# Kernel optimization log

Hardware: AMD Instinct MI355X
Metric: run time of the kernel (lower is better)

The kernel has to match this reference:

```python
import jax, jax.numpy as jnp
import numpy as np

EMB = 768
HEADS = 4
HEAD_DIM = EMB // HEADS


def setup_inputs() -> dict:
    key = jax.random.key(0)
    ks = jax.random.split(key, 11)
    B, S = 8, 2048
    scale = 1.0 / np.sqrt(EMB)
    inp = {
        "q": jax.random.normal(ks[0], (B, S, EMB), dtype=jnp.float32),
        "k": jax.random.normal(ks[1], (B, S, EMB), dtype=jnp.float32),
        "v": jax.random.normal(ks[2], (B, S, EMB), dtype=jnp.float32),
        "Wq": jax.random.normal(ks[3], (EMB, EMB), dtype=jnp.float32) * scale,
        "bq": jnp.zeros((EMB,), dtype=jnp.float32),
        "Wk": jax.random.normal(ks[4], (EMB, EMB), dtype=jnp.float32) * scale,
        "bk": jnp.zeros((EMB,), dtype=jnp.float32),
        "Wv": jax.random.normal(ks[5], (EMB, EMB), dtype=jnp.float32) * scale,
        "bv": jnp.zeros((EMB,), dtype=jnp.float32),
        "Wo": jax.random.normal(ks[6], (EMB, EMB), dtype=jnp.float32) * scale,
        "bo": jnp.zeros((EMB,), dtype=jnp.float32),
    }
    return inp


def reference(q, k, v, Wq, bq, Wk, bk, Wv, bv, Wo, bo):
    B, S, _ = q.shape
    # Linear projections (torch Linear: x @ W.T + b)
    Q = q @ Wq.T + bq
    K = k @ Wk.T + bk
    V = v @ Wv.T + bv
    # split heads: [B, H, S, Dh]
    def split(x):
        return x.reshape(B, S, HEADS, HEAD_DIM).transpose(0, 2, 1, 3)
    Qh, Kh, Vh = split(Q), split(K), split(V)
    # energy [B, H, S, S]; note: original's mask_fill is a non-inplace no-op, so no masking
    energy = jnp.einsum("bhqd,bhkd->bhqk", Qh, Kh)
    att = jax.nn.softmax(energy / jnp.sqrt(jnp.float32(HEAD_DIM)), axis=-1)
    # dropout p=0 -> identity
    out = jnp.einsum("bhqk,bhkd->bhqd", att, Vh)
    out = out.transpose(0, 2, 1, 3).reshape(B, S, EMB)
    return out @ Wo.T + bo
```

## Files before the change

kernel.cpp:

```cpp
#include <hip/hip_runtime.h>
#include <hip/hip_bf16.h>
#include <cstdint>
#include <cstddef>

#define EMB   768
#define HEADS 4
#define HD    192
#define BATCH 8
#define SEQ   2048
#define MROWS (BATCH * SEQ)

typedef __attribute__((ext_vector_type(8))) short bf16x8;
typedef __attribute__((ext_vector_type(4))) float f32x4;

#define GLOBAL_AS __attribute__((address_space(1)))
#define LDS_AS    __attribute__((address_space(3)))

__device__ __forceinline__ void async16(unsigned short* lds, const unsigned short* g) {
    __builtin_amdgcn_global_load_lds((const GLOBAL_AS void*)g, (LDS_AS void*)lds, 16, 0, 0);
}

__device__ __forceinline__ unsigned short f2bf(float f) {
    union { float f; unsigned int u; } v; v.f = f;
    unsigned int u = v.u;
    unsigned int r = u + 0x7fffu + ((u >> 16) & 1u);
    return (unsigned short)(r >> 16);
}

__device__ __forceinline__ unsigned long long pack4bf(float4 f) {
    union { __hip_bfloat162 h; unsigned int u; } a, b;
    a.h = __float22bfloat162_rn(make_float2(f.x, f.y));
    b.h = __float22bfloat162_rn(make_float2(f.z, f.w));
    return (unsigned long long)a.u | ((unsigned long long)b.u << 32);
}

__device__ __forceinline__ int swz(int colbyte, int row) {
    return colbyte ^ ((row & 7) << 4);
}

__global__ __launch_bounds__(256) void conv_kernel(
    const float* __restrict__ x, unsigned short* __restrict__ y, int n4)
{
    int i = blockIdx.x * 256 + threadIdx.x;
    int stride = gridDim.x * 256;
    for (; i < n4; i += stride) {
        float4 f = ((const float4*)x)[i];
        ((unsigned long long*)y)[i] = pack4bf(f);
    }
}

__global__ __launch_bounds__(256) void conv3_kernel(
    const float* __restrict__ a, const float* __restrict__ b,
    const float* __restrict__ c, unsigned short* __restrict__ y, int n4)
{
    int i = blockIdx.x * 256 + threadIdx.x;
    int stride = gridDim.x * 256;
    for (; i < 3 * n4; i += stride) {
        int sel = i / n4, off = i - sel * n4;
        const float* s = (sel == 0) ? a : (sel == 1) ? b : c;
        float4 f = ((const float4*)s)[off];
        ((unsigned long long*)y)[i] = pack4bf(f);
    }
}

#define GEMM_PROLOG                                                          \
    const int tid  = threadIdx.x;                                            \
    const int n0   = blockIdx.x * 128;                                       \
    const int m0   = blockIdx.y * 128;                                       \
    const int w    = tid >> 6;                                               \
    const int lane = tid & 63;                                               \
    const int l15  = lane & 15;                                              \
    const int quad = lane >> 4;                                              \
    const int wm   = (w >> 1) * 64;                                          \
    const int wn   = (w & 1) * 64;                                           \
    const int arow = lane >> 2;           \
    const int acol = (lane & 3) * 8;                  \
    f32x4 acc[4][4];                                                         \
    _Pragma("unroll")                                                        \
    for (int a = 0; a < 4; a++)                                              \
        _Pragma("unroll")                                                    \
        for (int b = 0; b < 4; b++) acc[a][b] = (f32x4)0.0f;

#define GEMM_KLOOP(Aptr, Bptr)                                               \
    for (int k0 = 0; k0 < 768; k0 += 32) {                                   \
        __syncthreads();                                                     \
        _Pragma("unroll")                                                    \
        for (int j = 0; j < 2; j++) {                                        \
            int r = w * 32 + j * 16 + arow;                                  \
            async16(&Al[(w * 2 + j) * 512],                                  \
                    Aptr + (size_t)(m0 + r) * 768 + k0 + acol);              \
            async16(&Bl[(w * 2 + j) * 512],                                  \
                    Bptr + (size_t)(n0 + r) * 768 + k0 + acol);              \
        }                                                                    \
        __syncthreads();                                                     \
        bf16x8 af[4], bfr[4];                                                \
        _Pragma("unroll")                                                    \
        for (int mi = 0; mi < 4; mi++)                                       \
            af[mi] = *(const bf16x8*)&Al[(wm + mi * 16 + l15) * 32 + quad * 8]; \
        _Pragma("unroll")                                                    \
        for (int ni = 0; ni < 4; ni++)                                       \
            bfr[ni] = *(const bf16x8*)&Bl[(wn + ni * 16 + l15) * 32 + quad * 8]; \
        _Pragma("unroll")                                                    \
        for (int mi = 0; mi < 4; mi++)                                       \
            _Pragma("unroll")                                                \
            for (int ni = 0; ni < 4; ni++)                                   \
                acc[mi][ni] = __builtin_amdgcn_mfma_f32_16x16x32_bf16(       \
                    af[mi], bfr[ni], acc[mi][ni], 0, 0, 0);                  \
    }

__global__ __launch_bounds__(256) void proj_kernel(
    const unsigned short* __restrict__ X,
    const unsigned short* __restrict__ Wb,
    const float* __restrict__ bias,
    unsigned short* __restrict__ out,
    float scale)
{
    __shared__ __align__(16) unsigned short Al[128 * 32];
    __shared__ __align__(16) unsigned short Bl[128 * 32];
    GEMM_PROLOG
    GEMM_KLOOP(X, Wb)

    const int b = m0 >> 11;
#pragma unroll
    for (int mi = 0; mi < 4; mi++) {
#pragma unroll
        for (int ni = 0; ni < 4; ni++) {
            int jj = n0 + wn + ni * 16 + l15;
            int h  = jj / HD;
            int d  = jj - h * HD;
            float bj = bias[jj];
#pragma unroll
            for (int r = 0; r < 4; r++) {
                int i = m0 + wm + mi * 16 + quad * 4 + r;
                int s = i & (SEQ - 1);
                out[(size_t)((b * HEADS + h) * SEQ + s) * HD + d] =
                    f2bf((acc[mi][ni][r] + bj) * scale);
            }
        }
    }
}

__global__ __launch_bounds__(256) void vproj_kernel(
    const unsigned short* __restrict__ X,
    const unsigned short* __restrict__ Wb,
    const float* __restrict__ bias,
    unsigned short* __restrict__ out)
{
    __shared__ __align__(16) unsigned short smem[8192];
    unsigned short* Al = smem;
    unsigned short* Bl = smem + 4096;
    GEMM_PROLOG
    GEMM_KLOOP(X, Wb)

    __syncthreads();
    unsigned short* Tl = smem;
    const int batch = m0 >> 11;
    const int s0    = m0 & (SEQ - 1);

#pragma unroll
    for (int g = 0; g < 4; g++) {
        if ((w & 1) == (g >> 1)) {
#pragma unroll
            for (int t = 0; t < 2; t++) {
                int ni = (g & 1) * 2 + t;
                int jj = n0 + (w & 1) * 64 + ni * 16 + l15;
                int dl = t * 16 + l15;
                float bj = bias[jj];
#pragma unroll
                for (int mi = 0; mi < 4; mi++)
#pragma unroll
                    for (int r = 0; r < 4; r++)
                        Tl[dl * 136 + wm + mi * 16 + quad * 4 + r] =
                            f2bf(acc[mi][ni][r] + bj);
            }
        }
        __syncthreads();
#pragma unroll
        for (int t = 0; t < 2; t++) {
            int u  = tid + t * 256;
            int dl = u >> 4;
            int cg = u & 15;
            int jj = n0 + g * 32 + dl;
            int hh = jj / HD;
            int d  = jj - hh * HD;
            *(int4*)(out + ((size_t)((batch * HEADS + hh) * HD + d)) * SEQ + s0 + cg * 8) =
                *(const int4*)&Tl[dl * 136 + cg * 8];
        }
        __syncthreads();
    }
}

__global__ __launch_bounds__(256) void oproj_kernel(
    const unsigned short* __restrict__ A,
    const unsigned short* __restrict__ Wb,
    const float* __restrict__ bias,
    float* __restrict__ out)
{
    __shared__ __align__(16) unsigned short Al[128 * 32];
    __shared__ __align__(16) unsigned short Bl[128 * 32];
    GEMM_PROLOG
    GEMM_KLOOP(A, Wb)

#pragma unroll
    for (int mi = 0; mi < 4; mi++) {
#pragma unroll
        for (int ni = 0; ni < 4; ni++) {
            int jj = n0 + wn + ni * 16 + l15;
            float bj = bias[jj];
#pragma unroll
            for (int r = 0; r < 4; r++) {
                int i = m0 + wm + mi * 16 + quad * 4 + r;
                out[(size_t)i * 768 + jj] = acc[mi][ni][r] + bj;
            }
        }
    }
}

__global__ __launch_bounds__(256, 2) void attn_kernel(
    const unsigned short* __restrict__ Q,
    const unsigned short* __restrict__ K,
    const unsigned short* __restrict__ Vt,
    unsigned short* __restrict__ O)
{
    __shared__ __align__(16) unsigned short Kl[64 * 192];
    __shared__ __align__(16) unsigned short Vl[192 * 64];
    __shared__ __align__(16) unsigned short Pl[4 * 32 * 64];

    const int tid  = threadIdx.x;
    const int w    = tid >> 6;
    const int lane = tid & 63;
    const int l15  = lane & 15;
    const int quad = lane >> 4;
    const int flat = blockIdx.x;
    const int loc  = flat >> 3;
    const int bh   = (flat & 7) * 4 + (loc >> 4);
    const int qt   = loc & 15;
    const int b    = bh >> 2;
    const int h    = bh & 3;
    const size_t kbase = (size_t)bh * SEQ * HD;

    bf16x8 qf[2][6];
    {
        const unsigned short* qp =
            Q + kbase + (size_t)(qt * 128 + w * 32 + l15) * HD + quad * 8;
#pragma unroll
        for (int mg = 0; mg < 2; mg++)
#pragma unroll
            for (int kk = 0; kk < 6; kk++)
                qf[mg][kk] = *(const bf16x8*)(qp + mg * 16 * HD + kk * 32);
    }

#pragma unroll
    for (int i = 0; i < 6; i++) {
        int u = tid + i * 256;
        int row = u / 24, rem = u - row * 24;
        int cgp = rem ^ (row & 7);
        async16(&Kl[(i * 256 + w * 64) * 8],
                K + kbase + (size_t)row * HD + cgp * 8);
    }

    f32x4 oacc[2][12];
#pragma unroll
    for (int mg = 0; mg < 2; mg++)
#pragma unroll
        for (int i = 0; i < 12; i++) oacc[mg][i] = (f32x4)0.0f;
    float lacc[2][4] = {{0.f, 0.f, 0.f, 0.f}, {0.f, 0.f, 0.f, 0.f}};

    for (int kt = 0; kt < SEQ / 64; kt++) {
        __syncthreads();

#pragma unroll
        for (int i = 0; i < 6; i++) {
            int u = tid + i * 256;
            int row = u >> 3;
            int cgp = (u & 7) ^ (row & 7);
            async16(&Vl[(i * 256 + w * 64) * 8],
                    Vt + kbase + (size_t)row * SEQ + kt * 64 + cgp * 8);
        }

        f32x4 sacc[2][4];
#pragma unroll
        for (int mg = 0; mg < 2; mg++)
#pragma unroll
            for (int nj = 0; nj < 4; nj++) sacc[mg][nj] = (f32x4)0.0f;

        __builtin_amdgcn_s_setprio(1);
#pragma unroll
        for (int kk = 0; kk < 6; kk++) {
#pragma unroll
            for (int nj = 0; nj < 4; nj++) {
                int row = nj * 16 + l15;
                bf16x8 bfr = *(const bf16x8*)((const char*)Kl + row * 384 +
                                              swz(kk * 64 + quad * 16, row));
                sacc[0][nj] = __builtin_amdgcn_mfma_f32_16x16x32_bf16(
                    qf[0][kk], bfr, sacc[0][nj], 0, 0, 0);
                sacc[1][nj] = __builtin_amdgcn_mfma_f32_16x16x32_bf16(
                    qf[1][kk], bfr, sacc[1][nj], 0, 0, 0);
            }
        }
        __builtin_amdgcn_s_setprio(0);

        {
            char* pw = (char*)Pl + w * 4096;
#pragma unroll
            for (int mg = 0; mg < 2; mg++)
#pragma unroll
                for (int nj = 0; nj < 4; nj++) {
                    int colb = (nj * 16 + l15) * 2;
#pragma unroll
                    for (int r = 0; r < 4; r++) {
                        float pv = __expf(sacc[mg][nj][r]);
                        lacc[mg][r] += pv;
                        int row = mg * 16 + quad * 4 + r;
                        *(unsigned short*)(pw + row * 128 + swz(colb, row)) = f2bf(pv);
                    }
                }
        }

        __syncthreads();

        {
            int ktn = (kt + 1) & (SEQ / 64 - 1);
#pragma unroll
            for (int i = 0; i < 6; i++) {
                int u = tid + i * 256;
                int row = u / 24, rem = u - row * 24;
                int cgp = rem ^ (row & 7);
                async16(&Kl[(i * 256 + w * 64) * 8],
                        K + kbase + (size_t)(ktn * 64 + row) * HD + cgp * 8);
            }
        }

#pragma unroll
        for (int kk = 0; kk < 2; kk++) {
            const char* pr = (const char*)Pl + w * 4096;
            bf16x8 pa0 = *(const bf16x8*)(pr + l15 * 128 + swz(kk * 64 + quad * 16, l15));
            bf16x8 pa1 = *(const bf16x8*)(pr + (16 + l15) * 128 + swz(kk * 64 + quad * 16, 16 + l15));
            __builtin_amdgcn_s_setprio(1);
#pragma unroll
            for (int nf = 0; nf < 12; nf++) {
                int vrow = nf * 16 + l15;
                bf16x8 vb = *(const bf16x8*)((const char*)Vl + vrow * 128 +
                                             swz(kk * 64 + quad * 16, vrow));
                oacc[0][nf] = __builtin_amdgcn_mfma_f32_16x16x32_bf16(pa0, vb, oacc[0][nf], 0, 0, 0);
                oacc[1][nf] = __builtin_amdgcn_mfma_f32_16x16x32_bf16(pa1, vb, oacc[1][nf], 0, 0, 0);
            }
            __builtin_amdgcn_s_setprio(0);
        }
    }

    float inv[2][4];
#pragma unroll
    for (int mg = 0; mg < 2; mg++)
#pragma unroll
        for (int r = 0; r < 4; r++) {
            float lsum = lacc[mg][r];
#pragma unroll
            for (int off = 1; off < 16; off <<= 1)
                lsum += __shfl_xor(lsum, off, 64);
            inv[mg][r] = 1.0f / lsum;
        }
#pragma unroll
    for (int mg = 0; mg < 2; mg++)
#pragma unroll
        for (int nf = 0; nf < 12; nf++) {
            int col = h * HD + nf * 16 + l15;
#pragma unroll
            for (int r = 0; r < 4; r++) {
                int s = qt * 128 + w * 32 + mg * 16 + quad * 4 + r;
                O[(size_t)(b * SEQ + s) * EMB + col] = f2bf(oacc[mg][nf][r] * inv[mg][r]);
            }
        }
}

extern "C" void kernel_launch(void* const* d_in, const int* in_sizes, int n_in,
                              void* d_out, int out_size, void* d_ws, size_t ws_size,
                              hipStream_t stream)
{
    const float* q  = (const float*)d_in[0];
    const float* k  = (const float*)d_in[1];
    const float* v  = (const float*)d_in[2];
    const float* Wq = (const float*)d_in[3];
    const float* bq = (const float*)d_in[4];
    const float* Wk = (const float*)d_in[5];
    const float* bk = (const float*)d_in[6];
    const float* Wv = (const float*)d_in[7];
    const float* bv = (const float*)d_in[8];
    const float* Wo = (const float*)d_in[9];
    const float* bo = (const float*)d_in[10];
    float* out = (float*)d_out;

    unsigned short* Xbf = (unsigned short*)d_out;
    unsigned short* S   = (unsigned short*)d_ws;
    unsigned short* Qb  = S  + (size_t)MROWS * EMB;
    unsigned short* Kb  = Qb + (size_t)MROWS * EMB;
    unsigned short* Vb  = Kb + (size_t)MROWS * EMB;
    const size_t WSZ = (size_t)EMB * EMB;

    const float scl = 0.07216878364870323f;
    const int   nx4 = MROWS * EMB / 4;
    const int   nw4 = EMB * EMB / 4;

    dim3 pb(256);
    dim3 pg(EMB / 128, MROWS / 128);
    dim3 cgx(4096), cgw(576);

    conv3_kernel<<<dim3(1728), pb, 0, stream>>>(Wq, Wk, Wv, S, nw4);

    conv_kernel<<<cgx, pb, 0, stream>>>(q, Xbf, nx4);
    proj_kernel<<<pg, pb, 0, stream>>>(Xbf, S, bq, Qb, scl);

    conv_kernel<<<cgx, pb, 0, stream>>>(k, Xbf, nx4);
    proj_kernel<<<pg, pb, 0, stream>>>(Xbf, S + WSZ, bk, Kb, 1.0f);

    conv_kernel<<<cgx, pb, 0, stream>>>(v, Xbf, nx4);
    vproj_kernel<<<pg, pb, 0, stream>>>(Xbf, S + 2 * WSZ, bv, Vb);

    dim3 ag(512);
    attn_kernel<<<ag, pb, 0, stream>>>(Qb, Kb, Vb, S);

    conv_kernel<<<cgw, pb, 0, stream>>>(Wo, Qb, nw4);
    oproj_kernel<<<pg, pb, 0, stream>>>(S, Qb, bo, out);
}
```

Before: 486.9 us.

## Double-buffer GEMM LDS tiles and remap blocks for XCD locality

```diff
diff --git a/kernel.cpp b/kernel.cpp
--- a/kernel.cpp
+++ b/kernel.cpp
@@ -65,8 +65,9 @@
 
 #define GEMM_PROLOG                                                          \
     const int tid  = threadIdx.x;                                            \
-    const int n0   = blockIdx.x * 128;                                       \
-    const int m0   = blockIdx.y * 128;                                       \
+    const int wg   = (blockIdx.x & 7) * 96 + (blockIdx.x >> 3);              \
+    const int n0   = (wg % 6) * 128;                                         \
+    const int m0   = (wg / 6) * 128;                                         \
     const int w    = tid >> 6;                                               \
     const int lane = tid & 63;                                               \
     const int l15  = lane & 15;                                              \
@@ -81,25 +82,27 @@
         _Pragma("unroll")                                                    \
         for (int b = 0; b < 4; b++) acc[a][b] = (f32x4)0.0f;
 
-#define GEMM_KLOOP(Aptr, Bptr)                                               \
-    for (int k0 = 0; k0 < 768; k0 += 32) {                                   \
-        __syncthreads();                                                     \
-        _Pragma("unroll")                                                    \
-        for (int j = 0; j < 2; j++) {                                        \
-            int r = w * 32 + j * 16 + arow;                                  \
-            async16(&Al[(w * 2 + j) * 512],                                  \
-                    Aptr + (size_t)(m0 + r) * 768 + k0 + acol);              \
-            async16(&Bl[(w * 2 + j) * 512],                                  \
-                    Bptr + (size_t)(n0 + r) * 768 + k0 + acol);              \
-        }                                                                    \
-        __syncthreads();                                                     \
+#define GEMM_STAGE(buf, Aptr, Bptr, k0)                                      \
+    _Pragma("unroll")                                                        \
+    for (int j = 0; j < 2; j++) {                                            \
+        int r = w * 32 + j * 16 + arow;                                      \
+        async16(&Al[(buf) * 4096 + (w * 2 + j) * 512],                       \
+                Aptr + (size_t)(m0 + r) * 768 + (k0) + acol);                \
+        async16(&Bl[(buf) * 4096 + (w * 2 + j) * 512],                       \
+                Bptr + (size_t)(n0 + r) * 768 + (k0) + acol);                \
+    }
+
+#define GEMM_COMPUTE(buf)                                                    \
+    {                                                                        \
         bf16x8 af[4], bfr[4];                                                \
         _Pragma("unroll")                                                    \
         for (int mi = 0; mi < 4; mi++)                                       \
-            af[mi] = *(const bf16x8*)&Al[(wm + mi * 16 + l15) * 32 + quad * 8]; \
+            af[mi] = *(const bf16x8*)&Al[(buf) * 4096 +                      \
+                                         (wm + mi * 16 + l15) * 32 + quad * 8]; \
         _Pragma("unroll")                                                    \
         for (int ni = 0; ni < 4; ni++)                                       \
-            bfr[ni] = *(const bf16x8*)&Bl[(wn + ni * 16 + l15) * 32 + quad * 8]; \
+            bfr[ni] = *(const bf16x8*)&Bl[(buf) * 4096 +                     \
+                                          (wn + ni * 16 + l15) * 32 + quad * 8]; \
         _Pragma("unroll")                                                    \
         for (int mi = 0; mi < 4; mi++)                                       \
             _Pragma("unroll")                                                \
@@ -108,6 +111,17 @@
                     af[mi], bfr[ni], acc[mi][ni], 0, 0, 0);                  \
     }
 
+#define GEMM_KLOOP(Aptr, Bptr)                                               \
+    GEMM_STAGE(0, Aptr, Bptr, 0)                                             \
+    for (int k0 = 0; k0 < 768; k0 += 64) {                                   \
+        __syncthreads();                                                     \
+        GEMM_STAGE(1, Aptr, Bptr, k0 + 32)                                   \
+        GEMM_COMPUTE(0)                                                      \
+        __syncthreads();                                                     \
+        if (k0 + 64 < 768) { GEMM_STAGE(0, Aptr, Bptr, k0 + 64) }            \
+        GEMM_COMPUTE(1)                                                      \
+    }
+
 __global__ __launch_bounds__(256) void proj_kernel(
     const unsigned short* __restrict__ X,
     const unsigned short* __restrict__ Wb,
@@ -115,8 +129,9 @@
     unsigned short* __restrict__ out,
     float scale)
 {
-    __shared__ __align__(16) unsigned short Al[128 * 32];
-    __shared__ __align__(16) unsigned short Bl[128 * 32];
+    __shared__ __align__(16) unsigned short smem[16384];
+    unsigned short* Al = smem;
+    unsigned short* Bl = smem + 8192;
     GEMM_PROLOG
     GEMM_KLOOP(X, Wb)
 
@@ -146,9 +161,9 @@
     const float* __restrict__ bias,
     unsigned short* __restrict__ out)
 {
-    __shared__ __align__(16) unsigned short smem[8192];
+    __shared__ __align__(16) unsigned short smem[16384];
     unsigned short* Al = smem;
-    unsigned short* Bl = smem + 4096;
+    unsigned short* Bl = smem + 8192;
     GEMM_PROLOG
     GEMM_KLOOP(X, Wb)
 
@@ -196,8 +211,9 @@
     const float* __restrict__ bias,
     float* __restrict__ out)
 {
-    __shared__ __align__(16) unsigned short Al[128 * 32];
-    __shared__ __align__(16) unsigned short Bl[128 * 32];
+    __shared__ __align__(16) unsigned short smem[16384];
+    unsigned short* Al = smem;
+    unsigned short* Bl = smem + 8192;
     GEMM_PROLOG
     GEMM_KLOOP(A, Wb)
 
@@ -402,7 +418,7 @@
     const int   nw4 = EMB * EMB / 4;
 
     dim3 pb(256);
-    dim3 pg(EMB / 128, MROWS / 128);
+    dim3 pg(768);
     dim3 cgx(4096), cgw(576);
 
     conv3_kernel<<<dim3(1728), pb, 0, stream>>>(Wq, Wk, Wv, S, nw4);
```

Result: faster. 475.7 us (-2.3%).
